# Performance work log

Hardware: AMD Instinct MI355X
Metric: run time of the kernel (lower is better)

Reference implementation:

```python
import jax, jax.numpy as jnp
import numpy as np

HIDDEN = [256, 128, 64, 32, 16]
INPUT_SIZE = 1


def _lstm_cell(x, h, c, w_ih, w_hh, b_ih, b_hh):
    # PyTorch LSTMCell: gates ordered (i, f, g, o)
    gates = x @ w_ih.T + h @ w_hh.T + b_ih + b_hh
    i, f, g, o = jnp.split(gates, 4, axis=-1)
    c_new = jax.nn.sigmoid(f) * c + jax.nn.sigmoid(i) * jnp.tanh(g)
    h_new = jax.nn.sigmoid(o) * jnp.tanh(c_new)
    return h_new, c_new


def setup_inputs() -> dict:
    key = jax.random.key(0)
    keys = iter(jax.random.split(key, 32))
    B, T = 128, 2048
    inp = {"inputData": jax.random.normal(next(keys), (B, T), dtype=jnp.float32)}
    in_sizes = [INPUT_SIZE] + HIDDEN[:-1]
    for li, (din, dh) in enumerate(zip(in_sizes, HIDDEN), start=1):
        inp[f"w{li}_ih"] = jax.random.normal(next(keys), (4 * dh, din), dtype=jnp.float32) * 0.05
        inp[f"w{li}_hh"] = jax.random.normal(next(keys), (4 * dh, dh), dtype=jnp.float32) * 0.05
        inp[f"b{li}_ih"] = jax.random.normal(next(keys), (4 * dh,), dtype=jnp.float32) * 0.05
        inp[f"b{li}_hh"] = jax.random.normal(next(keys), (4 * dh,), dtype=jnp.float32) * 0.05
    inp["w_lin"] = jax.random.normal(next(keys), (1, HIDDEN[-1]), dtype=jnp.float32) * 0.05
    inp["b_lin"] = jax.random.normal(next(keys), (1,), dtype=jnp.float32) * 0.05
    return inp


def reference(inputData,
              w1_ih, w1_hh, b1_ih, b1_hh,
              w2_ih, w2_hh, b2_ih, b2_hh,
              w3_ih, w3_hh, b3_ih, b3_hh,
              w4_ih, w4_hh, b4_ih, b4_hh,
              w5_ih, w5_hh, b5_ih, b5_hh,
              w_lin, b_lin):
    B = inputData.shape[0]
    params = [(w1_ih, w1_hh, b1_ih, b1_hh),
              (w2_ih, w2_hh, b2_ih, b2_hh),
              (w3_ih, w3_hh, b3_ih, b3_hh),
              (w4_ih, w4_hh, b4_ih, b4_hh),
              (w5_ih, w5_hh, b5_ih, b5_hh)]
    init_state = tuple((jnp.zeros((B, dh), inputData.dtype),
                        jnp.zeros((B, dh), inputData.dtype)) for dh in HIDDEN)

    xs = inputData.T[:, :, None]  # [T, B, 1]

    def step(state, x_t):
        new_state = []
        inp = x_t
        for (h, c), p in zip(state, params):
            h, c = _lstm_cell(inp, h, c, *p)
            new_state.append((h, c))
            inp = h
        out_t = inp @ w_lin.T + b_lin  # [B, 1]
        return tuple(new_state), out_t[:, 0]

    _, outs = jax.lax.scan(step, init_state, xs)  # outs: [T, B]
    return outs.T  # [B, T]
```

## Files before the change

### kernel.cpp

```cpp
#include <hip/hip_runtime.h>
#include <math.h>

#define TT 2048
#define NSLOT 6

#define FB_OFF  786432
#define ZERO_F4 49664

#define M0_X   65536
#define M1_LW3 49152
#define M1_X   73728
#define LDS_BYTES 149504

typedef _Float16 half2v __attribute__((ext_vector_type(2)));
typedef _Float16 half4v __attribute__((ext_vector_type(4)));
typedef _Float16 half8v __attribute__((ext_vector_type(8)));
typedef unsigned long long u64;
typedef unsigned int u32;

#if defined(__has_builtin)
#if __has_builtin(__builtin_amdgcn_fdot2)
#define HAVE_FDOT2 1
#endif
#endif

__device__ __forceinline__ float fdot2f(half2v a, half2v b, float c) {
#ifdef HAVE_FDOT2
    return __builtin_amdgcn_fdot2(a, b, c, false);
#else
    return c + (float)a.x * (float)b.x + (float)a.y * (float)b.y;
#endif
}
__device__ __forceinline__ half2v h2at(half8v v, int m) {
    half2v r; r.x = v[2 * m]; r.y = v[2 * m + 1]; return r;
}
__device__ __forceinline__ float dot8(half8v w, half8v x, float a) {
#pragma unroll
    for (int m = 0; m < 4; ++m) a = fdot2f(h2at(w, m), h2at(x, m), a);
    return a;
}
__device__ __forceinline__ half2v h2lo(half4v v) { half2v r; r.x = v[0]; r.y = v[1]; return r; }
__device__ __forceinline__ half2v h2hi(half4v v) { half2v r; r.x = v[2]; r.y = v[3]; return r; }

__device__ __forceinline__ float sigf(float x) { return 1.0f / (1.0f + __expf(-x)); }
__device__ __forceinline__ float tanh_f(float x) {
    float t = __expf(fminf(2.0f * x, 30.0f));
    return (t - 1.0f) / (t + 1.0f);
}
template<int CTRL, int XM>
__device__ __forceinline__ float xadd(float v) {
#if __has_builtin(__builtin_amdgcn_mov_dpp)
    int t = __builtin_amdgcn_mov_dpp(__builtin_bit_cast(int, v), CTRL, 0xF, 0xF, true);
    return v + __builtin_bit_cast(float, t);
#else
    return v + __shfl_xor(v, XM, 64);
#endif
}
__device__ __forceinline__ float xadd4(float v) {
#if __has_builtin(__builtin_amdgcn_ds_swizzle)
    int t = __builtin_amdgcn_ds_swizzle(__builtin_bit_cast(int, v), 0x101F);
    return v + __builtin_bit_cast(float, t);
#else
    return v + __shfl_xor(v, 4, 64);
#endif
}
__device__ __forceinline__ _Float16 lstm_fin(float g0, float g1, float g2, float g3, float& c) {
    float ig = sigf(g0), fg = sigf(g1), gg = tanh_f(g2), og = sigf(g3);
    float cn = fmaf(fg, c, ig * gg); c = cn;
    return (_Float16)(og * tanh_f(cn));
}
__device__ __forceinline__ int aload(const int* p) {
    return __hip_atomic_load((int*)p, __ATOMIC_RELAXED, __HIP_MEMORY_SCOPE_AGENT);
}
__device__ __forceinline__ void apost(int* p, int v) {
    __hip_atomic_store(p, v, __ATOMIC_RELAXED, __HIP_MEMORY_SCOPE_AGENT);
}
__device__ __forceinline__ u64 aload64(const u64* p) {
    return __hip_atomic_load((u64*)p, __ATOMIC_RELAXED, __HIP_MEMORY_SCOPE_AGENT);
}
__device__ __forceinline__ void astore64(u64* p, u64 v) {
    __hip_atomic_store(p, v, __ATOMIC_RELAXED, __HIP_MEMORY_SCOPE_AGENT);
}

__global__ __launch_bounds__(256)
void prep_zero(float4* ws) {
    int idx = blockIdx.x * 256 + threadIdx.x;
    if (idx < ZERO_F4) ws[idx] = make_float4(0.f, 0.f, 0.f, 0.f);
}

__global__ __launch_bounds__(512, 1)
void lstm_v8(const float* __restrict__ inp,
             const float* __restrict__ w1ih, const float* __restrict__ w1hh,
             const float* __restrict__ b1ih, const float* __restrict__ b1hh,
             const float* __restrict__ w2ih, const float* __restrict__ w2hh,
             const float* __restrict__ b2ih, const float* __restrict__ b2hh,
             const float* __restrict__ w3ih, const float* __restrict__ w3hh,
             const float* __restrict__ b3ih, const float* __restrict__ b3hh,
             const float* __restrict__ w4ih, const float* __restrict__ w4hh,
             const float* __restrict__ b4ih, const float* __restrict__ b4hh,
             const float* __restrict__ w5ih, const float* __restrict__ w5hh,
             const float* __restrict__ b5ih, const float* __restrict__ b5hh,
             const float* __restrict__ wlin, const float* __restrict__ blin,
             float* __restrict__ out, char* __restrict__ wsb)
{
    extern __shared__ __align__(16) _Float16 smem[];
    const int tid  = threadIdx.x;
    const int lane = tid & 63;
    const int wave = tid >> 6;
    const int g = blockIdx.x >> 1;
    u64* board = (u64*)wsb;
    int* fBp = (int*)(wsb + FB_OFF) + g * 16;

    if ((blockIdx.x & 1) == 0) {
        _Float16* lw = smem;
        _Float16* X0 = smem + M0_X;
        const int kg = tid & 3, slot = tid >> 2;
        const int du = kg & 1;

        half8v w[6][8];
#pragma unroll
        for (int r = 0; r < 6; ++r) {
            const int grow = (r >> 1) * 256 + slot * 2 + (r & 1);
#pragma unroll
            for (int j = 0; j < 8; ++j) {
                half8v t;
#pragma unroll
                for (int e = 0; e < 8; ++e)
                    t[e] = (_Float16)w1hh[grow * 256 + kg * 64 + j * 8 + e];
                w[r][j] = t;
            }
        }
        for (int rr = 0; rr < 2; ++rr) {
            const int grow = 3 * 256 + slot * 2 + rr;
            for (int e = 0; e < 64; ++e)
                lw[(size_t)((rr * 8 + (e >> 3)) * 512 + tid) * 8 + (e & 7)] =
                    (_Float16)w1hh[grow * 256 + kg * 64 + e];
        }
        float b4[4], wx4[4];
#pragma unroll
        for (int gg = 0; gg < 4; ++gg) {
            const int gr = gg * 256 + slot * 2 + du;
            b4[gg] = b1ih[gr] + b1hh[gr];
            wx4[gg] = w1ih[gr];
        }
        for (int i = tid; i < 512; i += 512) X0[i] = (_Float16)0.f;
        __syncthreads();

        float c1 = 0.f;
        float xcur = inp[(size_t)g * TT];
        int fc = 0, fnew = 0;
        const _Float16* lwp = lw + tid * 8;

        for (int s = 0; s <= 2048; ++s) {
            const int ph = s & 1, nph = ph ^ 1;

            if (wave == 0 && s >= 1) {
                if (s >= 7 && fc < s - 5) {
                    do { fc = aload(fBp); } while (fc < s - 5);
                }
                u64 hv = *(const u64*)(X0 + ph * 256 + lane * 4);
                u64* dst = board + ((size_t)((s - 1) % NSLOT) * 128 + g) * 128 + lane * 2;
                const u64 tg = (u64)(u32)s << 32;
                astore64(dst,     (hv & 0xffffffffull) | tg);
                astore64(dst + 1, (hv >> 32)           | tg);
                fnew = aload(fBp);
            }

            if (s < 2048) {
                const float xt = xcur;
                if (s + 1 < 2048) xcur = inp[(size_t)g * TT + s + 1];
                float acc[8];
#pragma unroll
                for (int r = 0; r < 8; ++r) acc[r] = 0.f;
#pragma unroll
                for (int c = 0; c < 8; ++c) {
                    const half8v xa = *(const half8v*)(X0 + ph * 256 + kg * 64 + c * 8);
#pragma unroll
                    for (int r = 0; r < 6; ++r)
                        acc[r] = dot8(w[r][c], xa, acc[r]);
                    const half8v la = *(const half8v*)(lwp + c * 4096);
                    acc[6] = dot8(la, xa, acc[6]);
                    const half8v ma = *(const half8v*)(lwp + 32768 + c * 4096);
                    acc[7] = dot8(ma, xa, acc[7]);
                }
#pragma unroll
                for (int r = 0; r < 8; ++r) {
                    float a = acc[r];
                    a = xadd<0xB1, 1>(a);
                    a = xadd<0x4E, 2>(a);
                    acc[r] = a;
                }
                if (kg < 2) {
                    float g0 = fmaf(wx4[0], xt, acc[0 + kg] + b4[0]);
                    float g1 = fmaf(wx4[1], xt, acc[2 + kg] + b4[1]);
                    float g2 = fmaf(wx4[2], xt, acc[4 + kg] + b4[2]);
                    float g3 = fmaf(wx4[3], xt, acc[6 + kg] + b4[3]);
                    X0[nph * 256 + slot * 2 + kg] = lstm_fin(g0, g1, g2, g3, c1);
                }
            }
            __syncthreads();
            if (fnew > fc) fc = fnew;
        }
        return;
    }

    _Float16* lw2 = smem;
    _Float16* lw3 = smem + M1_LW3;
    _Float16* X1  = smem + M1_X;
    const int kg = tid & 3;
    const int unit2 = tid >> 2;
    const int unit3 = tid >> 3;
    const int sub = (tid >> 2) & 1;

    half8v w2[3][12];
#pragma unroll
    for (int r = 0; r < 3; ++r) {
        const int grow = r * 128 + unit2;
#pragma unroll
        for (int j = 0; j < 12; ++j) {
            half8v t;
#pragma unroll
            for (int e = 0; e < 8; ++e) {
                const int k = kg * 96 + j * 8 + e;
                t[e] = (_Float16)((k < 256) ? w2ih[grow * 256 + k]
                                            : w2hh[grow * 128 + (k - 256)]);
            }
            w2[r][j] = t;
        }
    }
    {
        const int grow = 3 * 128 + unit2;
        for (int e = 0; e < 96; ++e) {
            const int k = kg * 96 + e;
            lw2[(size_t)((e >> 3) * 512 + tid) * 8 + (e & 7)] =
                (_Float16)((k < 256) ? w2ih[grow * 256 + k]
                                     : w2hh[grow * 128 + (k - 256)]);
        }
    }
    half8v w3[6];
    {
        const int grow = (sub * 2) * 64 + unit3;
#pragma unroll
        for (int j = 0; j < 6; ++j) {
            half8v t;
            for (int e = 0; e < 8; ++e) {
                const int k = kg * 48 + j * 8 + e;
                t[e] = (_Float16)((k < 128) ? w3ih[grow * 128 + k]
                                            : w3hh[grow * 64 + (k - 128)]);
            }
            w3[j] = t;
        }
        const int grow1 = (sub * 2 + 1) * 64 + unit3;
        for (int e = 0; e < 48; ++e) {
            const int k = kg * 48 + e;
            lw3[(size_t)((e >> 3) * 512 + tid) * 8 + (e & 7)] =
                (_Float16)((k < 128) ? w3ih[grow1 * 128 + k]
                                     : w3hh[grow1 * 64 + (k - 128)]);
        }
    }
    half2v wt[4][6];
    float bt[4] = {0.f, 0.f, 0.f, 0.f};
    if (tid >= 128 && tid < 384) {
        const int l = tid - 128, unit4 = l >> 3, kg8 = l & 7;
#pragma unroll
        for (int gg = 0; gg < 4; ++gg) {
            const int grow = gg * 32 + unit4;
#pragma unroll
            for (int m = 0; m < 6; ++m) {
                half2v t;
                for (int e = 0; e < 2; ++e) {
                    const int k = kg8 * 12 + m * 2 + e;
                    t[e] = (_Float16)((k < 64) ? w4ih[grow * 64 + k]
                                               : w4hh[grow * 32 + (k - 64)]);
                }
                wt[gg][m] = t;
            }
            bt[gg] = b4ih[grow] + b4hh[grow];
        }
    } else if (tid >= 384 && tid < 448) {
        const int l = tid - 384, unit5 = l >> 2, kg5 = l & 3;
#pragma unroll
        for (int gg = 0; gg < 4; ++gg) {
            const int grow = gg * 16 + unit5;
#pragma unroll
            for (int m = 0; m < 6; ++m) {
                half2v t;
                for (int e = 0; e < 2; ++e) {
                    const int k = kg5 * 12 + m * 2 + e;
                    t[e] = (_Float16)((k < 32) ? w5ih[grow * 32 + k]
                                               : w5hh[grow * 16 + (k - 32)]);
                }
                wt[gg][m] = t;
            }
            bt[gg] = b5ih[grow] + b5hh[grow];
        }
    }
    float b2v[4], b3v[4];
#pragma unroll
    for (int gg = 0; gg < 4; ++gg) {
        b2v[gg] = b2ih[gg * 128 + unit2] + b2hh[gg * 128 + unit2];
        b3v[gg] = b3ih[gg * 64 + unit3] + b3hh[gg * 64 + unit3];
    }
    float wlj = 0.f, blv = 0.f;
    if (tid >= 448 && tid < 464) { wlj = wlin[tid - 448]; blv = blin[0]; }

    for (int i = tid; i < 1024; i += 512) X1[i] = (_Float16)0.f;
    __syncthreads();
    if (wave == 7) {
        const u64* src = board + (size_t)g * 128 + 2 * lane;
        u64 a, b;
        do { a = aload64(src); b = aload64(src + 1); }
        while (!__all(((u32)(a >> 32) == 1u) && ((u32)(b >> 32) == 1u)));
        *(u64*)(X1 + 4 * lane) = (u64)(u32)a | ((u64)(u32)b << 32);
    }
    __syncthreads();

    float c2 = 0.f, c3 = 0.f, ct = 0.f;
    for (int t = 0; t <= 2051; ++t) {
        const int ph = t & 1, nph = ph ^ 1;
        u64 pa = 0, pb = 0;
        const bool dopf = (t + 1 <= 2047);
        const u64* psrc = board + ((size_t)((t + 1) % NSLOT) * 128 + g) * 128 + 2 * lane;
        if (wave == 7 && dopf) { pa = aload64(psrc); pb = aload64(psrc + 1); }

        if (t <= 2047) {
            float a0 = 0.f, a1 = 0.f, a2 = 0.f, a3 = 0.f;
#pragma unroll
            for (int c = 0; c < 12; ++c) {
                const half8v xa = *(const half8v*)(X1 + ph * 512 + kg * 96 + c * 8);
                a0 = dot8(w2[0][c], xa, a0);
                a1 = dot8(w2[1][c], xa, a1);
                a2 = dot8(w2[2][c], xa, a2);
                const half8v la = *(const half8v*)(lw2 + (size_t)(c * 512 + tid) * 8);
                a3 = dot8(la, xa, a3);
            }
            a0 = xadd<0xB1,1>(a0); a0 = xadd<0x4E,2>(a0);
            a1 = xadd<0xB1,1>(a1); a1 = xadd<0x4E,2>(a1);
            a2 = xadd<0xB1,1>(a2); a2 = xadd<0x4E,2>(a2);
            a3 = xadd<0xB1,1>(a3); a3 = xadd<0x4E,2>(a3);
            if (kg == 0)
                X1[nph * 512 + 256 + unit2] =
                    lstm_fin(a0 + b2v[0], a1 + b2v[1], a2 + b2v[2], a3 + b2v[3], c2);
        }
        if (t >= 1 && t <= 2048) {
            float sA = 0.f, sB = 0.f;
#pragma unroll
            for (int c = 0; c < 6; ++c) {
                const half8v xa = *(const half8v*)(X1 + ph * 512 + 256 + kg * 48 + c * 8);
                sA = dot8(w3[c], xa, sA);
                const half8v la = *(const half8v*)(lw3 + (size_t)(c * 512 + tid) * 8);
                sB = dot8(la, xa, sB);
            }
            sA = xadd<0xB1,1>(sA); sA = xadd<0x4E,2>(sA);
            sB = xadd<0xB1,1>(sB); sB = xadd<0x4E,2>(sB);
            const float sA2 = __shfl_xor(sA, 4, 64);
            const float sB2 = __shfl_xor(sB, 4, 64);
            if (kg == 0 && sub == 0)
                X1[nph * 512 + 384 + unit3] =
                    lstm_fin(sA + b3v[0], sB + b3v[1], sA2 + b3v[2], sB2 + b3v[3], c3);
        }
        if (tid >= 128 && tid < 384 && t >= 2 && t <= 2049) {
            const int l = tid - 128, kg8 = l & 7, unit4 = l >> 3;
            const _Float16* xp = X1 + ph * 512 + 384 + kg8 * 12;
            const half4v x0 = *(const half4v*)(xp);
            const half4v x1 = *(const half4v*)(xp + 4);
            const half4v x2 = *(const half4v*)(xp + 8);
            float a[4] = {0.f, 0.f, 0.f, 0.f};
#pragma unroll
            for (int gg = 0; gg < 4; ++gg) {
                a[gg] = fdot2f(wt[gg][0], h2lo(x0), a[gg]);
                a[gg] = fdot2f(wt[gg][1], h2hi(x0), a[gg]);
                a[gg] = fdot2f(wt[gg][2], h2lo(x1), a[gg]);
                a[gg] = fdot2f(wt[gg][3], h2hi(x1), a[gg]);
                a[gg] = fdot2f(wt[gg][4], h2lo(x2), a[gg]);
                a[gg] = fdot2f(wt[gg][5], h2hi(x2), a[gg]);
            }
#pragma unroll
            for (int gg = 0; gg < 4; ++gg) {
                float v = a[gg];
                v = xadd<0xB1,1>(v); v = xadd<0x4E,2>(v); v = xadd4(v);
                a[gg] = v;
            }
            if (kg8 == 0)
                X1[nph * 512 + 448 + unit4] =
                    lstm_fin(a[0] + bt[0], a[1] + bt[1], a[2] + bt[2], a[3] + bt[3], ct);
        }
        if (tid >= 384 && tid < 448 && t >= 3 && t <= 2050) {
            const int l = tid - 384, kg5 = l & 3, unit5 = l >> 2;
            const _Float16* xp = X1 + ph * 512 + 448 + kg5 * 12;
            const half4v x0 = *(const half4v*)(xp);
            const half4v x1 = *(const half4v*)(xp + 4);
            const half4v x2 = *(const half4v*)(xp + 8);
            float a[4] = {0.f, 0.f, 0.f, 0.f};
#pragma unroll
            for (int gg = 0; gg < 4; ++gg) {
                a[gg] = fdot2f(wt[gg][0], h2lo(x0), a[gg]);
                a[gg] = fdot2f(wt[gg][1], h2hi(x0), a[gg]);
                a[gg] = fdot2f(wt[gg][2], h2lo(x1), a[gg]);
                a[gg] = fdot2f(wt[gg][3], h2hi(x1), a[gg]);
                a[gg] = fdot2f(wt[gg][4], h2lo(x2), a[gg]);
                a[gg] = fdot2f(wt[gg][5], h2hi(x2), a[gg]);
            }
#pragma unroll
            for (int gg = 0; gg < 4; ++gg) {
                float v = a[gg];
                v = xadd<0xB1,1>(v); v = xadd<0x4E,2>(v);
                a[gg] = v;
            }
            if (kg5 == 0)
                X1[nph * 512 + 480 + unit5] =
                    lstm_fin(a[0] + bt[0], a[1] + bt[1], a[2] + bt[2], a[3] + bt[3], ct);
        }
        if (wave == 7 && lane < 16 && t >= 4) {
            float p = wlj * (float)X1[ph * 512 + 480 + lane];
            p += __shfl_xor(p, 1, 64); p += __shfl_xor(p, 2, 64);
            p += __shfl_xor(p, 4, 64); p += __shfl_xor(p, 8, 64);
            if (lane == 0) out[(size_t)g * TT + (t - 4)] = p + blv;
        }
        if (wave == 7 && dopf) {
            const u32 want = (u32)(t + 2);
            while (!__all(((u32)(pa >> 32) == want) && ((u32)(pb >> 32) == want))) {
                pa = aload64(psrc); pb = aload64(psrc + 1);
            }
            *(u64*)(X1 + nph * 512 + 4 * lane) = (u64)(u32)pa | ((u64)(u32)pb << 32);
            if (lane == 0) apost(fBp, t + 2);
        }
        __syncthreads();
    }
}

extern "C" void kernel_launch(void* const* d_in, const int* in_sizes, int n_in,
                              void* d_out, int out_size, void* d_ws, size_t ws_size,
                              hipStream_t stream) {
    const float* p[23];
    for (int i = 0; i < 23 && i < n_in; ++i) p[i] = (const float*)d_in[i];

    (void)hipFuncSetAttribute((const void*)lstm_v8,
                              hipFuncAttributeMaxDynamicSharedMemorySize,
                              LDS_BYTES);

    prep_zero<<<dim3((ZERO_F4 + 255) / 256), dim3(256), 0, stream>>>((float4*)d_ws);

    lstm_v8<<<dim3(256), dim3(512), LDS_BYTES, stream>>>(
        p[0],
        p[1],  p[2],  p[3],  p[4],
        p[5],  p[6],  p[7],  p[8],
        p[9],  p[10], p[11], p[12],
        p[13], p[14], p[15], p[16],
        p[17], p[18], p[19], p[20],
        p[21], p[22],
        (float*)d_out, (char*)d_ws);
}
```

Measured before the change: 6.282 ms.

## Switch layer-1 and layer-2 recurrent matvecs to MFMA 16x16x32 f16

Replaces the per-thread fdot2 matvec plus cross-lane reductions for LSTM layers 1 and 2 with MFMA 16x16x32 f16 instructions. Weights are held as MFMA A-fragments in registers, with the remainder spilled to LDS. Gate pre-activations go through a new LDS buffer and a one-thread-per-unit finish phase. The MFMA uses only one useful column of the B operand (a matrix-vector product), so most of the MFMA work is wasted. It also adds an extra __syncthreads per timestep in both blocks, which lengthens the serial recurrence critical path.

```diff
diff --git a/kernel.cpp b/kernel.cpp
--- a/kernel.cpp
+++ b/kernel.cpp
@@ -7,14 +7,17 @@
 #define FB_OFF  786432
 #define ZERO_F4 49664
 
-#define M0_X   65536
-#define M1_LW3 49152
-#define M1_X   73728
-#define LDS_BYTES 149504
+#define M0_X    73728
+#define M0_G    74240
+#define M1_LW3  49152
+#define M1_X    73728
+#define M1_G    74752
+#define LDS_BYTES 153600
 
 typedef _Float16 half2v __attribute__((ext_vector_type(2)));
 typedef _Float16 half4v __attribute__((ext_vector_type(4)));
 typedef _Float16 half8v __attribute__((ext_vector_type(8)));
+typedef float f32x4 __attribute__((ext_vector_type(4)));
 typedef unsigned long long u64;
 typedef unsigned int u32;
 
@@ -56,14 +59,6 @@
     return v + __shfl_xor(v, XM, 64);
 #endif
 }
-__device__ __forceinline__ float xadd4(float v) {
-#if __has_builtin(__builtin_amdgcn_ds_swizzle)
-    int t = __builtin_amdgcn_ds_swizzle(__builtin_bit_cast(int, v), 0x101F);
-    return v + __builtin_bit_cast(float, t);
-#else
-    return v + __shfl_xor(v, 4, 64);
-#endif
-}
 __device__ __forceinline__ _Float16 lstm_fin(float g0, float g1, float g2, float g3, float& c) {
     float ig = sigf(g0), fg = sigf(g1), gg = tanh_f(g2), og = sigf(g3);
     float cn = fmaf(fg, c, ig * gg); c = cn;
@@ -82,6 +77,10 @@
     __hip_atomic_store(p, v, __ATOMIC_RELAXED, __HIP_MEMORY_SCOPE_AGENT);
 }
 
+__device__ __forceinline__ int kmap(int lane, int e) {
+    return ((lane >> 4) << 2) + (e & 3) + ((e >> 2) << 4);
+}
+
 __global__ __launch_bounds__(256)
 void prep_zero(float4* ws) {
     int idx = blockIdx.x * 256 + threadIdx.x;
@@ -89,7 +88,7 @@
 }
 
 __global__ __launch_bounds__(512, 1)
-void lstm_v8(const float* __restrict__ inp,
+void lstm_v9(const float* __restrict__ inp,
              const float* __restrict__ w1ih, const float* __restrict__ w1hh,
              const float* __restrict__ b1ih, const float* __restrict__ b1hh,
              const float* __restrict__ w2ih, const float* __restrict__ w2hh,
@@ -110,38 +109,37 @@
     const int g = blockIdx.x >> 1;
     u64* board = (u64*)wsb;
     int* fBp = (int*)(wsb + FB_OFF) + g * 16;
+    const int lrow = lane & 15;
+    const int lblk = lane >> 4;
 
     if ((blockIdx.x & 1) == 0) {
-        _Float16* lw = smem;
+        _Float16* A1lds = smem;
         _Float16* X0 = smem + M0_X;
-        const int kg = tid & 3, slot = tid >> 2;
-        const int du = kg & 1;
-
-        half8v w[6][8];
-#pragma unroll
-        for (int r = 0; r < 6; ++r) {
-            const int grow = (r >> 1) * 256 + slot * 2 + (r & 1);
-#pragma unroll
-            for (int j = 0; j < 8; ++j) {
-                half8v t;
+        float*    G1 = (float*)(smem + M0_G);
+
+        half8v Areg[46];
+#pragma unroll
+        for (int j = 0; j < 8; ++j) {
+            const int rt = wave * 8 + j;
+            const int grow = (rt >> 4) * 256 + (rt & 15) * 16 + lrow;
+#pragma unroll
+            for (int kt = 0; kt < 8; ++kt) {
+                half8v a;
 #pragma unroll
                 for (int e = 0; e < 8; ++e)
-                    t[e] = (_Float16)w1hh[grow * 256 + kg * 64 + j * 8 + e];
-                w[r][j] = t;
-            }
-        }
-        for (int rr = 0; rr < 2; ++rr) {
-            const int grow = 3 * 256 + slot * 2 + rr;
-            for (int e = 0; e < 64; ++e)
-                lw[(size_t)((rr * 8 + (e >> 3)) * 512 + tid) * 8 + (e & 7)] =
-                    (_Float16)w1hh[grow * 256 + kg * 64 + e];
-        }
-        float b4[4], wx4[4];
-#pragma unroll
-        for (int gg = 0; gg < 4; ++gg) {
-            const int gr = gg * 256 + slot * 2 + du;
-            b4[gg] = b1ih[gr] + b1hh[gr];
-            wx4[gg] = w1ih[gr];
+                    a[e] = (_Float16)w1hh[grow * 256 + kt * 32 + kmap(lane, e)];
+                const int fi = j * 8 + kt;
+                if (fi < 46) Areg[fi < 46 ? fi : 0] = a;
+                else *(half8v*)(A1lds + ((size_t)(fi - 46) * 512 + tid) * 8) = a;
+            }
+        }
+        float b4[4] = {0.f,0.f,0.f,0.f}, wx4[4] = {0.f,0.f,0.f,0.f};
+        if (tid < 256) {
+#pragma unroll
+            for (int gg = 0; gg < 4; ++gg) {
+                b4[gg] = b1ih[gg * 256 + tid] + b1hh[gg * 256 + tid];
+                wx4[gg] = w1ih[gg * 256 + tid];
+            }
         }
         for (int i = tid; i < 512; i += 512) X0[i] = (_Float16)0.f;
         __syncthreads();
@@ -149,7 +147,6 @@
         float c1 = 0.f;
         float xcur = inp[(size_t)g * TT];
         int fc = 0, fnew = 0;
-        const _Float16* lwp = lw + tid * 8;
 
         for (int s = 0; s <= 2048; ++s) {
             const int ph = s & 1, nph = ph ^ 1;
@@ -166,37 +163,47 @@
                 fnew = aload(fBp);
             }
 
+            float xt = 0.f;
             if (s < 2048) {
-                const float xt = xcur;
+                xt = xcur;
                 if (s + 1 < 2048) xcur = inp[(size_t)g * TT + s + 1];
-                float acc[8];
-#pragma unroll
-                for (int r = 0; r < 8; ++r) acc[r] = 0.f;
-#pragma unroll
-                for (int c = 0; c < 8; ++c) {
-                    const half8v xa = *(const half8v*)(X0 + ph * 256 + kg * 64 + c * 8);
-#pragma unroll
-                    for (int r = 0; r < 6; ++r)
-                        acc[r] = dot8(w[r][c], xa, acc[r]);
-                    const half8v la = *(const half8v*)(lwp + c * 4096);
-                    acc[6] = dot8(la, xa, acc[6]);
-                    const half8v ma = *(const half8v*)(lwp + 32768 + c * 4096);
-                    acc[7] = dot8(ma, xa, acc[7]);
-                }
-#pragma unroll
-                for (int r = 0; r < 8; ++r) {
-                    float a = acc[r];
-                    a = xadd<0xB1, 1>(a);
-                    a = xadd<0x4E, 2>(a);
-                    acc[r] = a;
-                }
-                if (kg < 2) {
-                    float g0 = fmaf(wx4[0], xt, acc[0 + kg] + b4[0]);
-                    float g1 = fmaf(wx4[1], xt, acc[2 + kg] + b4[1]);
-                    float g2 = fmaf(wx4[2], xt, acc[4 + kg] + b4[2]);
-                    float g3 = fmaf(wx4[3], xt, acc[6 + kg] + b4[3]);
-                    X0[nph * 256 + slot * 2 + kg] = lstm_fin(g0, g1, g2, g3, c1);
-                }
+
+                f32x4 acc[8];
+#pragma unroll
+                for (int j = 0; j < 8; ++j) acc[j] = (f32x4){0.f,0.f,0.f,0.f};
+#pragma unroll
+                for (int kt = 0; kt < 8; ++kt) {
+                    half4v xlo = *(const half4v*)(X0 + ph * 256 + kt * 32 + lblk * 4);
+                    half4v xhi = *(const half4v*)(X0 + ph * 256 + kt * 32 + 16 + lblk * 4);
+                    half8v b;
+                    b[0]=xlo[0]; b[1]=xlo[1]; b[2]=xlo[2]; b[3]=xlo[3];
+                    b[4]=xhi[0]; b[5]=xhi[1]; b[6]=xhi[2]; b[7]=xhi[3];
+#pragma unroll
+                    for (int j = 0; j < 8; ++j) {
+                        const int fi = j * 8 + kt;
+                        half8v a;
+                        if (fi < 46) a = Areg[fi < 46 ? fi : 0];
+                        else a = *(const half8v*)(A1lds + ((size_t)(fi - 46) * 512 + tid) * 8);
+                        acc[j] = __builtin_amdgcn_mfma_f32_16x16x32_f16(a, b, acc[j], 0, 0, 0);
+                    }
+                }
+                if (lrow == 0) {
+#pragma unroll
+                    for (int j = 0; j < 8; ++j) {
+                        const int rt = wave * 8 + j;
+                        *(f32x4*)(G1 + (rt >> 4) * 256 + (rt & 15) * 16 + lblk * 4) = acc[j];
+                    }
+                }
+            }
+            __syncthreads();
+            if (s < 2048 && tid < 256) {
+                float g0 = G1[tid]       + b4[0];
+                float g1 = G1[256 + tid] + b4[1];
+                float g2 = G1[512 + tid] + b4[2];
+                float g3 = G1[768 + tid] + b4[3];
+                g0 = fmaf(wx4[0], xt, g0); g1 = fmaf(wx4[1], xt, g1);
+                g2 = fmaf(wx4[2], xt, g2); g3 = fmaf(wx4[3], xt, g3);
+                X0[nph * 256 + tid] = lstm_fin(g0, g1, g2, g3, c1);
             }
             __syncthreads();
             if (fnew > fc) fc = fnew;
@@ -204,39 +211,33 @@
         return;
     }
 
-    _Float16* lw2 = smem;
-    _Float16* lw3 = smem + M1_LW3;
-    _Float16* X1  = smem + M1_X;
+    _Float16* A2lds = smem;
+    _Float16* lw3  = smem + M1_LW3;
+    _Float16* X1   = smem + M1_X;
+    float*    G2   = (float*)(smem + M1_G);
+
+    half8v A2[36];
+#pragma unroll
+    for (int rtL = 0; rtL < 4; ++rtL) {
+        const int rt = wave * 4 + rtL;
+        const int grow = (rt >> 3) * 128 + (rt & 7) * 16 + lrow;
+#pragma unroll
+        for (int kt = 0; kt < 12; ++kt) {
+            half8v a;
+#pragma unroll
+            for (int e = 0; e < 8; ++e) {
+                const int k = kt * 32 + kmap(lane, e);
+                a[e] = (_Float16)((k < 256) ? w2ih[grow * 256 + k]
+                                            : w2hh[grow * 128 + (k - 256)]);
+            }
+            const int fi = rtL * 12 + kt;
+            if (fi < 36) A2[fi < 36 ? fi : 0] = a;
+            else *(half8v*)(A2lds + ((size_t)kt * 512 + tid) * 8) = a;
+        }
+    }
     const int kg = tid & 3;
-    const int unit2 = tid >> 2;
     const int unit3 = tid >> 3;
     const int sub = (tid >> 2) & 1;
-
-    half8v w2[3][12];
-#pragma unroll
-    for (int r = 0; r < 3; ++r) {
-        const int grow = r * 128 + unit2;
-#pragma unroll
-        for (int j = 0; j < 12; ++j) {
-            half8v t;
-#pragma unroll
-            for (int e = 0; e < 8; ++e) {
-                const int k = kg * 96 + j * 8 + e;
-                t[e] = (_Float16)((k < 256) ? w2ih[grow * 256 + k]
-                                            : w2hh[grow * 128 + (k - 256)]);
-            }
-            w2[r][j] = t;
-        }
-    }
-    {
-        const int grow = 3 * 128 + unit2;
-        for (int e = 0; e < 96; ++e) {
-            const int k = kg * 96 + e;
-            lw2[(size_t)((e >> 3) * 512 + tid) * 8 + (e & 7)] =
-                (_Float16)((k < 256) ? w2ih[grow * 256 + k]
-                                     : w2hh[grow * 128 + (k - 256)]);
-        }
-    }
     half8v w3[6];
     {
         const int grow = (sub * 2) * 64 + unit3;
@@ -295,12 +296,15 @@
             bt[gg] = b5ih[grow] + b5hh[grow];
         }
     }
-    float b2v[4], b3v[4];
-#pragma unroll
-    for (int gg = 0; gg < 4; ++gg) {
-        b2v[gg] = b2ih[gg * 128 + unit2] + b2hh[gg * 128 + unit2];
+    float b2v[4] = {0.f,0.f,0.f,0.f}, b3v[4];
+    if (tid < 128) {
+#pragma unroll
+        for (int gg = 0; gg < 4; ++gg)
+            b2v[gg] = b2ih[gg * 128 + tid] + b2hh[gg * 128 + tid];
+    }
+#pragma unroll
+    for (int gg = 0; gg < 4; ++gg)
         b3v[gg] = b3ih[gg * 64 + unit3] + b3hh[gg * 64 + unit3];
-    }
     float wlj = 0.f, blv = 0.f;
     if (tid >= 448 && tid < 464) { wlj = wlin[tid - 448]; blv = blin[0]; }
 
@@ -324,23 +328,32 @@
         if (wave == 7 && dopf) { pa = aload64(psrc); pb = aload64(psrc + 1); }
 
         if (t <= 2047) {
-            float a0 = 0.f, a1 = 0.f, a2 = 0.f, a3 = 0.f;
-#pragma unroll
-            for (int c = 0; c < 12; ++c) {
-                const half8v xa = *(const half8v*)(X1 + ph * 512 + kg * 96 + c * 8);
-                a0 = dot8(w2[0][c], xa, a0);
-                a1 = dot8(w2[1][c], xa, a1);
-                a2 = dot8(w2[2][c], xa, a2);
-                const half8v la = *(const half8v*)(lw2 + (size_t)(c * 512 + tid) * 8);
-                a3 = dot8(la, xa, a3);
-            }
-            a0 = xadd<0xB1,1>(a0); a0 = xadd<0x4E,2>(a0);
-            a1 = xadd<0xB1,1>(a1); a1 = xadd<0x4E,2>(a1);
-            a2 = xadd<0xB1,1>(a2); a2 = xadd<0x4E,2>(a2);
-            a3 = xadd<0xB1,1>(a3); a3 = xadd<0x4E,2>(a3);
-            if (kg == 0)
-                X1[nph * 512 + 256 + unit2] =
-                    lstm_fin(a0 + b2v[0], a1 + b2v[1], a2 + b2v[2], a3 + b2v[3], c2);
+            f32x4 acc[4];
+#pragma unroll
+            for (int r = 0; r < 4; ++r) acc[r] = (f32x4){0.f,0.f,0.f,0.f};
+#pragma unroll
+            for (int kt = 0; kt < 12; ++kt) {
+                half4v xlo = *(const half4v*)(X1 + ph * 512 + kt * 32 + lblk * 4);
+                half4v xhi = *(const half4v*)(X1 + ph * 512 + kt * 32 + 16 + lblk * 4);
+                half8v b;
+                b[0]=xlo[0]; b[1]=xlo[1]; b[2]=xlo[2]; b[3]=xlo[3];
+                b[4]=xhi[0]; b[5]=xhi[1]; b[6]=xhi[2]; b[7]=xhi[3];
+#pragma unroll
+                for (int rtL = 0; rtL < 4; ++rtL) {
+                    const int fi = rtL * 12 + kt;
+                    half8v a;
+                    if (fi < 36) a = A2[fi < 36 ? fi : 0];
+                    else a = *(const half8v*)(A2lds + ((size_t)kt * 512 + tid) * 8);
+                    acc[rtL] = __builtin_amdgcn_mfma_f32_16x16x32_f16(a, b, acc[rtL], 0, 0, 0);
+                }
+            }
+            if (lrow == 0) {
+#pragma unroll
+                for (int rtL = 0; rtL < 4; ++rtL) {
+                    const int rt = wave * 4 + rtL;
+                    *(f32x4*)(G2 + (rt >> 3) * 128 + (rt & 7) * 16 + lblk * 4) = acc[rtL];
+                }
+            }
         }
         if (t >= 1 && t <= 2048) {
             float sA = 0.f, sB = 0.f;
@@ -378,7 +391,8 @@
 #pragma unroll
             for (int gg = 0; gg < 4; ++gg) {
                 float v = a[gg];
-                v = xadd<0xB1,1>(v); v = xadd<0x4E,2>(v); v = xadd4(v);
+                v = xadd<0xB1,1>(v); v = xadd<0x4E,2>(v);
+                v += __shfl_xor(v, 4, 64);
                 a[gg] = v;
             }
             if (kg8 == 0)
@@ -417,6 +431,15 @@
             p += __shfl_xor(p, 4, 64); p += __shfl_xor(p, 8, 64);
             if (lane == 0) out[(size_t)g * TT + (t - 4)] = p + blv;
         }
+
+        __syncthreads();
+        if (t <= 2047 && tid < 128) {
+            float g0 = G2[tid]       + b2v[0];
+            float g1 = G2[128 + tid] + b2v[1];
+            float g2 = G2[256 + tid] + b2v[2];
+            float g3 = G2[384 + tid] + b2v[3];
+            X1[nph * 512 + 256 + tid] = lstm_fin(g0, g1, g2, g3, c2);
+        }
         if (wave == 7 && dopf) {
             const u32 want = (u32)(t + 2);
             while (!__all(((u32)(pa >> 32) == want) && ((u32)(pb >> 32) == want))) {
@@ -435,13 +458,13 @@
     const float* p[23];
     for (int i = 0; i < 23 && i < n_in; ++i) p[i] = (const float*)d_in[i];
 
-    (void)hipFuncSetAttribute((const void*)lstm_v8,
+    (void)hipFuncSetAttribute((const void*)lstm_v9,
                               hipFuncAttributeMaxDynamicSharedMemorySize,
                               LDS_BYTES);
 
     prep_zero<<<dim3((ZERO_F4 + 255) / 256), dim3(256), 0, stream>>>((float4*)d_ws);
 
-    lstm_v8<<<dim3(256), dim3(512), LDS_BYTES, stream>>>(
+    lstm_v9<<<dim3(256), dim3(512), LDS_BYTES, stream>>>(
         p[0],
         p[1],  p[2],  p[3],  p[4],
         p[5],  p[6],  p[7],  p[8],
```

Measured after the change: 5.691 ms. 9.4% less time.
